# Optimization experiments

Hardware: AMD Instinct MI355X
Metric: run time of the kernel (lower is better)

## Reference

```python
import jax, jax.numpy as jnp
import numpy as np

N = 10000          # nodes
E_RAND = 320000    # random edges (avg degree 32)
F_IN = 512         # nfeat
HID = 256          # args.hid
HEADS = 8          # args.head
FH = HID // HEADS  # 32 per head
NCLASS = 40
TAU = 0.5
LAMDA = 0.5
K = 2


def setup_inputs() -> dict:
    key = jax.random.key(0)
    ks = jax.random.split(key, 16)
    # edge list: random edges + self-loops (so every dst segment is non-empty)
    src = jnp.concatenate([jax.random.randint(ks[0], (E_RAND,), 0, N), jnp.arange(N)])
    dst = jnp.concatenate([jax.random.randint(ks[1], (E_RAND,), 0, N), jnp.arange(N)])
    s = 0.05  # small init scale keeps exp() in attention/bind_loss stable
    return {
        "x": jax.random.normal(ks[2], (N, F_IN), jnp.float32),
        "src": src, "dst": dst,
        "W0": jax.random.normal(ks[3], (F_IN, HEADS, FH), jnp.float32) * s,
        "a0s": jax.random.normal(ks[4], (HEADS, FH), jnp.float32) * s,
        "a0d": jax.random.normal(ks[5], (HEADS, FH), jnp.float32) * s,
        "W1": jax.random.normal(ks[6], (HID, HEADS, FH), jnp.float32) * s,
        "a1s": jax.random.normal(ks[7], (HEADS, FH), jnp.float32) * s,
        "a1d": jax.random.normal(ks[8], (HEADS, FH), jnp.float32) * s,
        "W2": jax.random.normal(ks[9], (HID, HEADS, FH), jnp.float32) * s,
        "a2s": jax.random.normal(ks[10], (HEADS, FH), jnp.float32) * s,
        "a2d": jax.random.normal(ks[11], (HEADS, FH), jnp.float32) * s,
        "Wout": jax.random.normal(ks[12], (HID, HEADS, NCLASS), jnp.float32) * s,
        "aos": jax.random.normal(ks[13], (HEADS, NCLASS), jnp.float32) * s,
        "aod": jax.random.normal(ks[14], (HEADS, NCLASS), jnp.float32) * s,
    }


def _gat_layer(x, W, a_s, a_d, src, dst):
    """Sparse multi-head GAT layer: gather -> edge softmax -> scatter."""
    n = x.shape[0]
    h = jnp.einsum('nf,fhd->nhd', x, W)              # [N,H,Fh]
    es = jnp.sum(h * a_s, axis=-1)                    # [N,H]
    ed = jnp.sum(h * a_d, axis=-1)                    # [N,H]
    e = jax.nn.leaky_relu(es[src] + ed[dst], 0.2)     # [E,H]
    m = jax.ops.segment_max(e, dst, num_segments=n)   # per-dst max (stable softmax)
    w = jnp.exp(e - m[dst])
    z = jax.ops.segment_sum(w, dst, num_segments=n)
    alpha = w / z[dst]                                # [E,H]
    return jax.ops.segment_sum(alpha[:, :, None] * h[src], dst, num_segments=n)  # [N,H,Fh]


def _bind_loss(z):
    # z1 == z2 == z in the original call site: refl_sim == between_sim
    zn = z / jnp.maximum(jnp.linalg.norm(z, axis=1, keepdims=True), 1e-12)
    S = jnp.exp(jnp.matmul(zn, zn.T) / TAU)           # [N,N]
    d = jnp.diagonal(S)
    off = jnp.sum(S, axis=1) - d                      # masked (off-diagonal) row sum
    CT = -jnp.log(d / (off + off))                    # neg_c2.sum + neg_c3.sum
    return jnp.mean(CT)


def reference(x, src, dst, W0, a0s, a0d, W1, a1s, a1d, W2, a2s, a2d, Wout, aos, aod):
    layers = [(W0, a0s, a0d), (W1, a1s, a1d), (W2, a2s, a2d)]
    last = x
    loss = jnp.float32(0.0)
    for i, (W, as_, ad_) in enumerate(layers):
        cur = jax.nn.elu(_gat_layer(last, W, as_, ad_, src, dst))
        cur = cur.reshape(cur.shape[0], -1)           # concat heads -> [N, HID]
        if i > 0:
            beta = LAMDA / (i + 2)                    # MaskLayer(last, cur, lamda, i+2)
            cur = beta * last + (1.0 - beta) * cur
            if i % K == 0:
                loss = loss + _bind_loss(cur)
        last = cur
    out = _gat_layer(last, Wout, aos, aod, src, dst).mean(axis=1)  # avg heads -> [N,C]
    return (jax.nn.log_softmax(out, axis=1), loss)
```

## Files before the change

### kernel.cpp

```cpp
#include <hip/hip_runtime.h>
#include <hip/hip_bf16.h>
#include <math.h>

#define NN_F_IN   512
#define NN_HID    256
#define NN_HEADS  8
#define NN_FH     32
#define NN_NCLASS 40
#define TAU_F     0.5f
#define LAMDA_F   0.5f

typedef __attribute__((ext_vector_type(8))) short bf16x8;
typedef __attribute__((ext_vector_type(4))) float f32x4;

static __device__ __forceinline__ float lrelu02(float x) { return x >= 0.f ? x : 0.2f * x; }
static __device__ __forceinline__ float elu1(float x)    { return x > 0.f ? x : expm1f(x); }
static __device__ __forceinline__ float b2f(unsigned short u) {
    unsigned int x = ((unsigned int)u) << 16;
    return __uint_as_float(x);
}
static __device__ __forceinline__ unsigned short f2b(float f) {
    __hip_bfloat16 hb = __float2bfloat16(f);
    return *reinterpret_cast<unsigned short*>(&hb);
}

__global__ void cast_f2b_kernel(const float* __restrict__ src,
                                unsigned short* __restrict__ dst, int n4) {
    int i = blockIdx.x * 256 + threadIdx.x;
    if (i >= n4) return;
    float4 v = *(const float4*)(src + (size_t)i * 4);
    ushort4 o;
    o.x = f2b(v.x); o.y = f2b(v.y); o.z = f2b(v.z); o.w = f2b(v.w);
    *(ushort4*)(dst + (size_t)i * 4) = o;
}

__global__ void castW_kernel(const float* __restrict__ W, unsigned short* __restrict__ Wt,
                             int K, int Nc, int Np) {
    int idx = blockIdx.x * 256 + threadIdx.x;
    if (idx >= Np * K) return;
    int np = idx / K, k = idx - np * K;
    float v = (np < Nc) ? W[(size_t)k * Nc + np] : 0.f;
    Wt[idx] = f2b(v);
}

__global__ __launch_bounds__(256) void fc_mfma(const unsigned short* __restrict__ A,
                                               const unsigned short* __restrict__ B,
                                               unsigned short* __restrict__ H,
                                               int M, int K, int ncols, int ldH) {
    int t = threadIdx.x, lane = t & 63, wid = t >> 6;
    int wrow = wid >> 1, wcol = wid & 1;
    int l15 = lane & 15, lg = lane >> 4;
    int mbase = blockIdx.y * 64 + wrow * 32;
    int nbase = blockIdx.x * 64 + wcol * 32;

    const unsigned short* Ap[2];
    const unsigned short* Bp[2];
#pragma unroll
    for (int m = 0; m < 2; ++m) {
        int rr = mbase + m * 16 + l15;
        if (rr > M - 1) rr = M - 1;
        Ap[m] = A + (size_t)rr * K + lg * 8;
        Bp[m] = B + (size_t)(nbase + m * 16 + l15) * K + lg * 8;
    }
    f32x4 acc[2][2];
#pragma unroll
    for (int m = 0; m < 2; ++m)
#pragma unroll
        for (int nn = 0; nn < 2; ++nn)
#pragma unroll
            for (int r = 0; r < 4; ++r) acc[m][nn][r] = 0.f;

    bf16x8 aP[2], bP[2], aQ[2], bQ[2];
#pragma unroll
    for (int m = 0; m < 2; ++m) {
        aP[m] = *(const bf16x8*)(Ap[m]);
        bP[m] = *(const bf16x8*)(Bp[m]);
    }
    int nhalf = K >> 6;
    int kk = 32;
    for (int it = 0; it < nhalf; ++it) {
#pragma unroll
        for (int m = 0; m < 2; ++m) {
            aQ[m] = *(const bf16x8*)(Ap[m] + kk);
            bQ[m] = *(const bf16x8*)(Bp[m] + kk);
        }
#pragma unroll
        for (int m = 0; m < 2; ++m)
#pragma unroll
            for (int nn = 0; nn < 2; ++nn)
                acc[m][nn] = __builtin_amdgcn_mfma_f32_16x16x32_bf16(aP[m], bP[nn], acc[m][nn], 0, 0, 0);
        if (it + 1 < nhalf) {
#pragma unroll
            for (int m = 0; m < 2; ++m) {
                aP[m] = *(const bf16x8*)(Ap[m] + kk + 32);
                bP[m] = *(const bf16x8*)(Bp[m] + kk + 32);
            }
        }
#pragma unroll
        for (int m = 0; m < 2; ++m)
#pragma unroll
            for (int nn = 0; nn < 2; ++nn)
                acc[m][nn] = __builtin_amdgcn_mfma_f32_16x16x32_bf16(aQ[m], bQ[nn], acc[m][nn], 0, 0, 0);
        kk += 64;
    }
#pragma unroll
    for (int m = 0; m < 2; ++m) {
#pragma unroll
        for (int nn = 0; nn < 2; ++nn) {
            int col = nbase + nn * 16 + l15;
            if (col >= ncols) continue;
#pragma unroll
            for (int r = 0; r < 4; ++r) {
                int row = mbase + m * 16 + lg * 4 + r;
                if (row < M) H[(size_t)row * ldH + col] = f2b(acc[m][nn][r]);
            }
        }
    }
}

__global__ void attn_kernel(const unsigned short* __restrict__ Hm, const float* __restrict__ As,
                            const float* __restrict__ Ad, float* __restrict__ es,
                            float* __restrict__ ed, int n, int df) {
    int idx = blockIdx.x * blockDim.x + threadIdx.x;
    if (idx >= n * NN_HEADS) return;
    int nn = idx / NN_HEADS, hh = idx - nn * NN_HEADS;
    const unsigned short* hp = Hm + (size_t)nn * NN_HEADS * df + hh * df;
    const float* ap = As + hh * df;
    const float* bp = Ad + hh * df;
    float s1 = 0.f, s2 = 0.f;
    for (int d = 0; d < df; d += 4) {
        ushort4 hv = *(const ushort4*)(hp + d);
        float4 av = *(const float4*)(ap + d);
        float4 bv = *(const float4*)(bp + d);
        float h0 = b2f(hv.x), h1 = b2f(hv.y), h2 = b2f(hv.z), h3 = b2f(hv.w);
        s1 += h0 * av.x + h1 * av.y + h2 * av.z + h3 * av.w;
        s2 += h0 * bv.x + h1 * bv.y + h2 * bv.z + h3 * bv.w;
    }
    es[idx] = s1;
    ed[idx] = s2;
}

__global__ __launch_bounds__(256) void edge_wz(
    const float* __restrict__ es, const float* __restrict__ ed,
    const int* __restrict__ csr_src, const int* __restrict__ row_start,
    float* __restrict__ wC, float* __restrict__ zinv, int n) {
    int lane = threadIdx.x & 63;
    int nn   = blockIdx.x * 4 + (threadIdx.x >> 6);
    if (nn >= n) return;
    int s0 = row_start[nn], s1 = row_start[nn + 1];
    int h    = lane & 7;
    int slot = lane >> 3;
    float edh = ed[nn * NN_HEADS + h];
    float z = 0.f;
    for (int e = s0 + slot; e < s1; e += 8) {
        int sv = csr_src[e];
        float w = expf(lrelu02(es[sv * NN_HEADS + h] + edh));
        wC[(size_t)e * NN_HEADS + h] = w;
        z += w;
    }
    z += __shfl_xor(z, 8, 64);
    z += __shfl_xor(z, 16, 64);
    z += __shfl_xor(z, 32, 64);
    if (slot == 0) zinv[nn * NN_HEADS + h] = 1.f / z;
}

__global__ void count_kernel(const int* __restrict__ dst, int* __restrict__ counts, int E) {
    int e = blockIdx.x * blockDim.x + threadIdx.x;
    if (e < E) atomicAdd(&counts[dst[e]], 1);
}

__global__ void scan_kernel(const int* __restrict__ counts, int* __restrict__ row_start,
                            int* __restrict__ cursor, int n) {
    __shared__ int s[1024];
    int t  = threadIdx.x;
    int ch = (n + 1023) / 1024;
    int lo = t * ch;
    int sum = 0;
    for (int j = 0; j < ch; ++j) {
        int i = lo + j;
        if (i < n) sum += counts[i];
    }
    s[t] = sum;
    __syncthreads();
    for (int off = 1; off < 1024; off <<= 1) {
        int v = 0;
        if (t >= off) v = s[t - off];
        __syncthreads();
        s[t] += v;
        __syncthreads();
    }
    int run = (t == 0) ? 0 : s[t - 1];
    for (int j = 0; j < ch; ++j) {
        int i = lo + j;
        if (i < n) {
            row_start[i] = run;
            cursor[i] = run;
            run += counts[i];
        }
    }
    if (t == 1023) row_start[n] = s[1023];
}

__global__ void scatter_kernel(const int* __restrict__ src, const int* __restrict__ dst,
                               int* __restrict__ cursor, int* __restrict__ csr_src, int E) {
    int e = blockIdx.x * blockDim.x + threadIdx.x;
    if (e < E) {
        int d   = dst[e];
        int pos = atomicAdd(&cursor[d], 1);
        csr_src[pos] = src[e];
    }
}

__global__ __launch_bounds__(256) void gather_hidden(
    const unsigned short* __restrict__ Hm, const float* __restrict__ wC,
    const float* __restrict__ zinv, const int* __restrict__ csr_src,
    const int* __restrict__ row_start, const unsigned short* __restrict__ last,
    unsigned short* __restrict__ out, int n, float beta) {
    int lane = threadIdx.x & 63;
    int nn   = blockIdx.x * 4 + (threadIdx.x >> 6);
    if (nn >= n) return;
    int s0 = row_start[nn], s1 = row_start[nn + 1];
    int h2 = lane >> 3;

    float a0 = 0.f, a1 = 0.f, a2 = 0.f, a3 = 0.f;
    for (int e = s0; e < s1; e += 8) {
        int c = s1 - e;
        int idx[8];
        float wv[8];
#pragma unroll
        for (int j = 0; j < 8; ++j) {
            int p = (j < c) ? e + j : e;
            idx[j] = csr_src[p];
            wv[j]  = wC[(size_t)p * NN_HEADS + h2];
        }
        ushort4 r[8];
#pragma unroll
        for (int j = 0; j < 8; ++j) r[j] = *(const ushort4*)&Hm[(size_t)idx[j] * NN_HID + lane * 4];
#pragma unroll
        for (int j = 0; j < 8; ++j) {
            if (j < c) {
                float w = wv[j];
                a0 += w * b2f(r[j].x); a1 += w * b2f(r[j].y);
                a2 += w * b2f(r[j].z); a3 += w * b2f(r[j].w);
            }
        }
    }
    float zi = zinv[nn * NN_HEADS + h2];
    float v0 = elu1(a0 * zi), v1 = elu1(a1 * zi), v2 = elu1(a2 * zi), v3 = elu1(a3 * zi);
    if (beta >= 0.f) {
        ushort4 lv = *(const ushort4*)&last[(size_t)nn * NN_HID + lane * 4];
        v0 = beta * b2f(lv.x) + (1.f - beta) * v0;
        v1 = beta * b2f(lv.y) + (1.f - beta) * v1;
        v2 = beta * b2f(lv.z) + (1.f - beta) * v2;
        v3 = beta * b2f(lv.w) + (1.f - beta) * v3;
    }
    ushort4 o;
    o.x = f2b(v0); o.y = f2b(v1); o.z = f2b(v2); o.w = f2b(v3);
    *(ushort4*)&out[(size_t)nn * NN_HID + lane * 4] = o;
}

__global__ void gather_final(const unsigned short* __restrict__ Hm, const float* __restrict__ wC,
                             const float* __restrict__ zinv, const int* __restrict__ csr_src,
                             const int* __restrict__ row_start, float* __restrict__ dout, int n) {
    int nn = blockIdx.x;
    __shared__ float accs[NN_HEADS * NN_NCLASS];
    int t = threadIdx.x;
    int s0 = row_start[nn], s1 = row_start[nn + 1];
    int hh = t / NN_NCLASS;
    float acc = 0.f;
    const int LD = NN_HEADS * NN_NCLASS;
    for (int e = s0; e < s1; e += 8) {
        int c = s1 - e;
        int idx[8];
        float wv[8];
#pragma unroll
        for (int j = 0; j < 8; ++j) {
            int p = (j < c) ? e + j : e;
            idx[j] = csr_src[p];
            wv[j]  = wC[(size_t)p * NN_HEADS + hh];
        }
        float v[8];
#pragma unroll
        for (int j = 0; j < 8; ++j) v[j] = b2f(Hm[(size_t)idx[j] * LD + t]);
#pragma unroll
        for (int j = 0; j < 8; ++j) {
            if (j < c) acc += wv[j] * v[j];
        }
    }
    accs[t] = acc * zinv[nn * NN_HEADS + hh];
    __syncthreads();
    if (t < 64) {
        float v = -INFINITY;
        if (t < NN_NCLASS) {
            float sacc = 0.f;
#pragma unroll
            for (int h2 = 0; h2 < NN_HEADS; ++h2) sacc += accs[h2 * NN_NCLASS + t];
            v = sacc * (1.f / NN_HEADS);
        }
        float mx = v;
#pragma unroll
        for (int o = 1; o < 64; o <<= 1) mx = fmaxf(mx, __shfl_xor(mx, o, 64));
        float ex = (t < NN_NCLASS) ? expf(v - mx) : 0.f;
        float se = ex;
#pragma unroll
        for (int o = 1; o < 64; o <<= 1) se += __shfl_xor(se, o, 64);
        if (t < NN_NCLASS) dout[(size_t)nn * NN_NCLASS + t] = (v - mx) - logf(se);
    }
}

__global__ void rownorm_kernel(const unsigned short* __restrict__ z, short* __restrict__ znb,
                               float* __restrict__ dvec, int n) {
    int nn = blockIdx.x;
    int t  = threadIdx.x;
    float v  = b2f(z[(size_t)nn * NN_HID + t]);
    float sq = v * v;
#pragma unroll
    for (int o = 1; o < 64; o <<= 1) sq += __shfl_xor(sq, o, 64);
    __shared__ float ws[4];
    if ((t & 63) == 0) ws[t >> 6] = sq;
    __syncthreads();
    float s = ws[0] + ws[1] + ws[2] + ws[3];
    float m = fmaxf(sqrtf(s), 1e-12f);
    znb[(size_t)nn * NN_HID + t] = (short)f2b(v / m);
    if (t == 0) dvec[nn] = expf((s / (m * m)) * (1.f / TAU_F));
}

__global__ __launch_bounds__(256) void gram_mfma(const short* __restrict__ znb,
                                                 float* __restrict__ P2d, int n,
                                                 int T, int nwg, int Npad) {
    __shared__ short As[128 * 64];
    __shared__ short Bs[128 * 64];

    int b = blockIdx.x;
    int q = nwg >> 3, r8 = nwg & 7, xc = b & 7, oo = b >> 3;
    int sid = (xc < r8 ? xc * (q + 1) : r8 * (q + 1) + (xc - r8) * q) + oo;
    int bi = 0, rem = sid;
    while (rem >= T - bi) { rem -= T - bi; ++bi; }
    int bj = bi + rem;
    int i0 = bi * 128, j0 = bj * 128;

    int t    = threadIdx.x;
    int lane = t & 63;
    int wid  = t >> 6;
    int wrow = wid >> 1, wcol = wid & 1;
    int l15  = lane & 15, lg = lane >> 4;
    int srow = lane >> 3;
    int sch  = lane & 7;

    f32x4 acc[4][4];
#pragma unroll
    for (int m = 0; m < 4; ++m)
#pragma unroll
        for (int nn = 0; nn < 4; ++nn)
#pragma unroll
            for (int r = 0; r < 4; ++r) acc[m][nn][r] = 0.f;

    bf16x8 sa[4], sb[4];
#pragma unroll
    for (int s = 0; s < 4; ++s) {
        int row = wid * 32 + s * 8 + srow;
        int gch = sch ^ (row & 7);
        sa[s] = *(const bf16x8*)(znb + (size_t)(i0 + row) * NN_HID + gch * 8);
        sb[s] = *(const bf16x8*)(znb + (size_t)(j0 + row) * NN_HID + gch * 8);
    }

#pragma unroll
    for (int kt = 0; kt < 4; ++kt) {
#pragma unroll
        for (int s = 0; s < 4; ++s) {
            int row = wid * 32 + s * 8 + srow;
            *(bf16x8*)(&As[row * 64 + sch * 8]) = sa[s];
            *(bf16x8*)(&Bs[row * 64 + sch * 8]) = sb[s];
        }
        __syncthreads();
        if (kt < 3) {
            int kb = (kt + 1) * 64;
#pragma unroll
            for (int s = 0; s < 4; ++s) {
                int row = wid * 32 + s * 8 + srow;
                int gch = sch ^ (row & 7);
                sa[s] = *(const bf16x8*)(znb + (size_t)(i0 + row) * NN_HID + kb + gch * 8);
                sb[s] = *(const bf16x8*)(znb + (size_t)(j0 + row) * NN_HID + kb + gch * 8);
            }
        }
#pragma unroll
        for (int ks = 0; ks < 2; ++ks) {
            bf16x8 av[4], bv[4];
#pragma unroll
            for (int m = 0; m < 4; ++m) {
                int Ra = wrow * 64 + m * 16 + l15;
                int Rb = wcol * 64 + m * 16 + l15;
                int ca = (ks * 4 + lg) ^ (Ra & 7);
                int cb = (ks * 4 + lg) ^ (Rb & 7);
                av[m] = *(const bf16x8*)(&As[Ra * 64 + ca * 8]);
                bv[m] = *(const bf16x8*)(&Bs[Rb * 64 + cb * 8]);
            }
#pragma unroll
            for (int m = 0; m < 4; ++m)
#pragma unroll
                for (int nn = 0; nn < 4; ++nn)
                    acc[m][nn] = __builtin_amdgcn_mfma_f32_16x16x32_bf16(av[m], bv[nn], acc[m][nn], 0, 0, 0);
        }
        __syncthreads();
    }

    int i0w = i0 + wrow * 64;
    int j0w = j0 + wcol * 64;
    bool diag = (bj == bi);
#pragma unroll
    for (int m = 0; m < 4; ++m)
#pragma unroll
        for (int nn = 0; nn < 4; ++nn) {
            int gj = j0w + nn * 16 + l15;
            bool jok = gj < n;
#pragma unroll
            for (int r = 0; r < 4; ++r) {
                int gi = i0w + m * 16 + lg * 4 + r;
                acc[m][nn][r] = (jok && gi < n) ? expf(acc[m][nn][r] * (1.f / TAU_F)) : 0.f;
            }
        }
    float* rowslot = P2d + (size_t)(2 * bj + wcol) * Npad;
#pragma unroll
    for (int m = 0; m < 4; ++m) {
#pragma unroll
        for (int r = 0; r < 4; ++r) {
            float v = acc[m][0][r] + acc[m][1][r] + acc[m][2][r] + acc[m][3][r];
            v += __shfl_xor(v, 1, 64);
            v += __shfl_xor(v, 2, 64);
            v += __shfl_xor(v, 4, 64);
            v += __shfl_xor(v, 8, 64);
            if (l15 == 0) {
                int gi = i0w + m * 16 + lg * 4 + r;
                if (gi < n) rowslot[gi] = v;
            }
        }
    }
    if (!diag) {
        float* colslot = P2d + (size_t)(2 * bi + wrow) * Npad;
#pragma unroll
        for (int nn = 0; nn < 4; ++nn) {
            float v = 0.f;
#pragma unroll
            for (int m = 0; m < 4; ++m)
#pragma unroll
                for (int r = 0; r < 4; ++r) v += acc[m][nn][r];
            v += __shfl_xor(v, 16, 64);
            v += __shfl_xor(v, 32, 64);
            if (lg == 0) {
                int gj = j0w + nn * 16 + l15;
                if (gj < n) colslot[gj] = v;
            }
        }
    }
}

__global__ void fold_kernel(const float* __restrict__ P2d, float* __restrict__ R,
                            int n, int slots, int Npad) {
    int i = blockIdx.x * 256 + threadIdx.x;
    if (i >= n) return;
    const float* p = P2d + i;
    float s0 = 0.f, s1 = 0.f, s2 = 0.f, s3 = 0.f;
    int sl = 0;
    for (; sl + 4 <= slots; sl += 4) {
        s0 += p[(size_t)(sl + 0) * Npad];
        s1 += p[(size_t)(sl + 1) * Npad];
        s2 += p[(size_t)(sl + 2) * Npad];
        s3 += p[(size_t)(sl + 3) * Npad];
    }
    for (; sl < slots; ++sl) s0 += p[(size_t)sl * Npad];
    R[i] = (s0 + s1) + (s2 + s3);
}

__global__ void loss_kernel(const float* __restrict__ R, const float* __restrict__ dvec,
                            float* __restrict__ out_loss, int n) {
    __shared__ float s[1024];
    int t = threadIdx.x;
    float sum = 0.f;
    for (int i = t; i < n; i += 1024) {
        float d   = dvec[i];
        float off = R[i] - d;
        sum += -logf(d / (off + off));
    }
    s[t] = sum;
    __syncthreads();
    for (int o = 512; o > 0; o >>= 1) {
        if (t < o) s[t] += s[t + o];
        __syncthreads();
    }
    if (t == 0) *out_loss = s[0] / n;
}

extern "C" void kernel_launch(void* const* d_in, const int* in_sizes, int n_in,
                              void* d_out, int out_size, void* d_ws, size_t ws_size,
                              hipStream_t stream) {
    const float* x   = (const float*)d_in[0];
    const int*   src = (const int*)d_in[1];
    const int*   dst = (const int*)d_in[2];
    const float* W0  = (const float*)d_in[3];
    const float* a0s = (const float*)d_in[4];
    const float* a0d = (const float*)d_in[5];
    const float* W1  = (const float*)d_in[6];
    const float* a1s = (const float*)d_in[7];
    const float* a1d = (const float*)d_in[8];
    const float* W2  = (const float*)d_in[9];
    const float* a2s = (const float*)d_in[10];
    const float* a2d = (const float*)d_in[11];
    const float* Wout= (const float*)d_in[12];
    const float* aos = (const float*)d_in[13];
    const float* aod = (const float*)d_in[14];

    int N = in_sizes[0] / NN_F_IN;
    int E = in_sizes[1];
    int Npad = ((N + 127) / 128) * 128;
    int T = Npad / 128;
    int nwg = T * (T + 1) / 2;
    float* out = (float*)d_out;

    char*  ws  = (char*)d_ws;
    size_t off = 0;
    auto alloc = [&](size_t bytes) -> void* {
        void* p = ws + off;
        off += bytes;
        off = (off + 255) & ~(size_t)255;
        return p;
    };
    size_t hbBytes = (size_t)N * 320 * 2;
    size_t znBytes = (size_t)Npad * NN_HID * 2;
    unsigned short* Hb = (unsigned short*)alloc(hbBytes > znBytes ? hbBytes : znBytes);
    short* znb = (short*)Hb;
    unsigned short* Bl = (unsigned short*)alloc((size_t)N * NN_HID * 2);
    unsigned short* Bc = (unsigned short*)alloc((size_t)N * NN_HID * 2);
    size_t xbBytes = (size_t)N * NN_F_IN * 2;
    size_t p2Bytes = (size_t)2 * T * Npad * 4;
    void* XbP2d = alloc(xbBytes > p2Bytes ? xbBytes : p2Bytes);
    unsigned short* Xb  = (unsigned short*)XbP2d;
    float*          P2d = (float*)XbP2d;
    unsigned short* Wt0 = (unsigned short*)alloc((size_t)256 * 512 * 2);
    unsigned short* Wt1 = (unsigned short*)alloc((size_t)256 * 256 * 2);
    unsigned short* Wt2 = (unsigned short*)alloc((size_t)256 * 256 * 2);
    unsigned short* Wto = (unsigned short*)alloc((size_t)384 * 256 * 2);
    float* es     = (float*)alloc((size_t)N * NN_HEADS * 4);
    float* ed     = (float*)alloc((size_t)N * NN_HEADS * 4);
    float* wC     = (float*)alloc((size_t)E * NN_HEADS * 4);
    float* zinvA  = (float*)alloc((size_t)N * NN_HEADS * 4);
    float* Rrow   = (float*)alloc((size_t)N * 4);
    float* dvec   = (float*)alloc((size_t)N * 4);
    int*   counts = (int*)alloc((size_t)N * 4);
    int*   rs     = (int*)alloc((size_t)(N + 1) * 4);
    int*   cursor = (int*)alloc((size_t)N * 4);
    int*   csr    = (int*)alloc((size_t)E * 4);

    hipMemsetAsync(counts, 0, (size_t)N * 4, stream);
    count_kernel<<<(E + 255) / 256, 256, 0, stream>>>(dst, counts, E);
    scan_kernel<<<1, 1024, 0, stream>>>(counts, rs, cursor, N);
    scatter_kernel<<<(E + 255) / 256, 256, 0, stream>>>(src, dst, cursor, csr, E);

    cast_f2b_kernel<<<(N * NN_F_IN / 4 + 255) / 256, 256, 0, stream>>>(x, Xb, N * NN_F_IN / 4);
    castW_kernel<<<(256 * 512 + 255) / 256, 256, 0, stream>>>(W0, Wt0, 512, 256, 256);
    castW_kernel<<<(256 * 256 + 255) / 256, 256, 0, stream>>>(W1, Wt1, 256, 256, 256);
    castW_kernel<<<(256 * 256 + 255) / 256, 256, 0, stream>>>(W2, Wt2, 256, 256, 256);
    castW_kernel<<<(384 * 256 + 255) / 256, 256, 0, stream>>>(Wout, Wto, 256, 320, 384);

    int atGrid = (N * NN_HEADS + 255) / 256;
    int ghGrid = (N + 3) / 4;
    int mT64 = (N + 63) / 64;

    fc_mfma<<<dim3(4, mT64), 256, 0, stream>>>(Xb, Wt0, Hb, N, 512, 256, 256);
    attn_kernel<<<atGrid, 256, 0, stream>>>(Hb, a0s, a0d, es, ed, N, NN_FH);
    edge_wz<<<ghGrid, 256, 0, stream>>>(es, ed, csr, rs, wC, zinvA, N);
    gather_hidden<<<ghGrid, 256, 0, stream>>>(Hb, wC, zinvA, csr, rs, nullptr, Bl, N, -1.f);

    fc_mfma<<<dim3(4, mT64), 256, 0, stream>>>(Bl, Wt1, Hb, N, 256, 256, 256);
    attn_kernel<<<atGrid, 256, 0, stream>>>(Hb, a1s, a1d, es, ed, N, NN_FH);
    edge_wz<<<ghGrid, 256, 0, stream>>>(es, ed, csr, rs, wC, zinvA, N);
    gather_hidden<<<ghGrid, 256, 0, stream>>>(Hb, wC, zinvA, csr, rs, Bl, Bc, N, LAMDA_F / 3.f);

    fc_mfma<<<dim3(4, mT64), 256, 0, stream>>>(Bc, Wt2, Hb, N, 256, 256, 256);
    attn_kernel<<<atGrid, 256, 0, stream>>>(Hb, a2s, a2d, es, ed, N, NN_FH);
    edge_wz<<<ghGrid, 256, 0, stream>>>(es, ed, csr, rs, wC, zinvA, N);
    gather_hidden<<<ghGrid, 256, 0, stream>>>(Hb, wC, zinvA, csr, rs, Bc, Bl, N, LAMDA_F / 4.f);

    rownorm_kernel<<<N, 256, 0, stream>>>(Bl, znb, dvec, N);
    hipMemsetAsync(znb + (size_t)N * NN_HID, 0, (size_t)(Npad - N) * NN_HID * 2, stream);
    hipMemsetAsync(P2d, 0, (size_t)2 * T * Npad * 4, stream);
    gram_mfma<<<nwg, 256, 0, stream>>>(znb, P2d, N, T, nwg, Npad);
    fold_kernel<<<(N + 255) / 256, 256, 0, stream>>>(P2d, Rrow, N, 2 * T, Npad);
    loss_kernel<<<1, 1024, 0, stream>>>(Rrow, dvec, out + (size_t)N * NN_NCLASS, N);

    fc_mfma<<<dim3(5, mT64), 256, 0, stream>>>(Bl, Wto, Hb, N, 256, 320, 320);
    attn_kernel<<<atGrid, 256, 0, stream>>>(Hb, aos, aod, es, ed, N, NN_NCLASS);
    edge_wz<<<ghGrid, 256, 0, stream>>>(es, ed, csr, rs, wC, zinvA, N);
    gather_final<<<N, NN_HEADS * NN_NCLASS, 0, stream>>>(Hb, wC, zinvA, csr, rs, out, N);
}
```

Baseline: 432.9 us.

## Fuse cast kernels, use fast exp, and widen gram K-tile to 128

Merges the five input/weight cast kernels into one prep kernel to cut launch overhead. Replaces expf with __expf in the edge weight, row-norm and gram epilogue paths. Doubles the gram kernel's shared-memory K tile from 64 to 128, halving the K iterations and barriers at the cost of twice the LDS per block, which may lower occupancy. Fast exp trades a little accuracy.

```diff
diff --git a/kernel.cpp b/kernel.cpp
--- a/kernel.cpp
+++ b/kernel.cpp
@@ -24,23 +24,44 @@
     return *reinterpret_cast<unsigned short*>(&hb);
 }
 
-__global__ void cast_f2b_kernel(const float* __restrict__ src,
-                                unsigned short* __restrict__ dst, int n4) {
+__global__ void prep_kernel(const float* __restrict__ x,
+                            const float* __restrict__ W0, const float* __restrict__ W1,
+                            const float* __restrict__ W2, const float* __restrict__ Wo,
+                            unsigned short* __restrict__ Xb,
+                            unsigned short* __restrict__ Wt0, unsigned short* __restrict__ Wt1,
+                            unsigned short* __restrict__ Wt2, unsigned short* __restrict__ Wto,
+                            int n4X) {
     int i = blockIdx.x * 256 + threadIdx.x;
-    if (i >= n4) return;
-    float4 v = *(const float4*)(src + (size_t)i * 4);
-    ushort4 o;
-    o.x = f2b(v.x); o.y = f2b(v.y); o.z = f2b(v.z); o.w = f2b(v.w);
-    *(ushort4*)(dst + (size_t)i * 4) = o;
-}
-
-__global__ void castW_kernel(const float* __restrict__ W, unsigned short* __restrict__ Wt,
-                             int K, int Nc, int Np) {
-    int idx = blockIdx.x * 256 + threadIdx.x;
-    if (idx >= Np * K) return;
-    int np = idx / K, k = idx - np * K;
-    float v = (np < Nc) ? W[(size_t)k * Nc + np] : 0.f;
-    Wt[idx] = f2b(v);
+    if (i < n4X) {
+        float4 v = *(const float4*)(x + (size_t)i * 4);
+        ushort4 o;
+        o.x = f2b(v.x); o.y = f2b(v.y); o.z = f2b(v.z); o.w = f2b(v.w);
+        *(ushort4*)(Xb + (size_t)i * 4) = o;
+        return;
+    }
+    i -= n4X;
+    if (i < 256 * 512) {
+        int np = i >> 9, k = i & 511;
+        Wt0[i] = f2b(W0[(size_t)k * 256 + np]);
+        return;
+    }
+    i -= 256 * 512;
+    if (i < 256 * 256) {
+        int np = i >> 8, k = i & 255;
+        Wt1[i] = f2b(W1[(size_t)k * 256 + np]);
+        return;
+    }
+    i -= 256 * 256;
+    if (i < 256 * 256) {
+        int np = i >> 8, k = i & 255;
+        Wt2[i] = f2b(W2[(size_t)k * 256 + np]);
+        return;
+    }
+    i -= 256 * 256;
+    if (i < 384 * 256) {
+        int np = i >> 8, k = i & 255;
+        Wto[i] = f2b(np < 320 ? Wo[(size_t)k * 320 + np] : 0.f);
+    }
 }
 
 __global__ __launch_bounds__(256) void fc_mfma(const unsigned short* __restrict__ A,
@@ -154,7 +175,7 @@
     float z = 0.f;
     for (int e = s0 + slot; e < s1; e += 8) {
         int sv = csr_src[e];
-        float w = expf(lrelu02(es[sv * NN_HEADS + h] + edh));
+        float w = __expf(lrelu02(es[sv * NN_HEADS + h] + edh));
         wC[(size_t)e * NN_HEADS + h] = w;
         z += w;
     }
@@ -322,14 +343,14 @@
     float s = ws[0] + ws[1] + ws[2] + ws[3];
     float m = fmaxf(sqrtf(s), 1e-12f);
     znb[(size_t)nn * NN_HID + t] = (short)f2b(v / m);
-    if (t == 0) dvec[nn] = expf((s / (m * m)) * (1.f / TAU_F));
+    if (t == 0) dvec[nn] = __expf((s / (m * m)) * (1.f / TAU_F));
 }
 
 __global__ __launch_bounds__(256) void gram_mfma(const short* __restrict__ znb,
                                                  float* __restrict__ P2d, int n,
                                                  int T, int nwg, int Npad) {
-    __shared__ short As[128 * 64];
-    __shared__ short Bs[128 * 64];
+    __shared__ short As[128 * 128];
+    __shared__ short Bs[128 * 128];
 
     int b = blockIdx.x;
     int q = nwg >> 3, r8 = nwg & 7, xc = b & 7, oo = b >> 3;
@@ -344,8 +365,8 @@
     int wid  = t >> 6;
     int wrow = wid >> 1, wcol = wid & 1;
     int l15  = lane & 15, lg = lane >> 4;
-    int srow = lane >> 3;
-    int sch  = lane & 7;
+    int sc16 = lane & 15;
+    int sr4  = lane >> 4;
 
     f32x4 acc[4][4];
 #pragma unroll
@@ -355,36 +376,35 @@
 #pragma unroll
             for (int r = 0; r < 4; ++r) acc[m][nn][r] = 0.f;
 
-    bf16x8 sa[4], sb[4];
-#pragma unroll
-    for (int s = 0; s < 4; ++s) {
-        int row = wid * 32 + s * 8 + srow;
-        int gch = sch ^ (row & 7);
+    bf16x8 sa[8], sb[8];
+#pragma unroll
+    for (int s = 0; s < 8; ++s) {
+        int row = wid * 32 + sr4 * 8 + s;
+        int gch = sc16 ^ (row & 7);
         sa[s] = *(const bf16x8*)(znb + (size_t)(i0 + row) * NN_HID + gch * 8);
         sb[s] = *(const bf16x8*)(znb + (size_t)(j0 + row) * NN_HID + gch * 8);
     }
 
 #pragma unroll
-    for (int kt = 0; kt < 4; ++kt) {
-#pragma unroll
-        for (int s = 0; s < 4; ++s) {
-            int row = wid * 32 + s * 8 + srow;
-            *(bf16x8*)(&As[row * 64 + sch * 8]) = sa[s];
-            *(bf16x8*)(&Bs[row * 64 + sch * 8]) = sb[s];
+    for (int kt = 0; kt < 2; ++kt) {
+#pragma unroll
+        for (int s = 0; s < 8; ++s) {
+            int row = wid * 32 + sr4 * 8 + s;
+            *(bf16x8*)(&As[row * 128 + sc16 * 8]) = sa[s];
+            *(bf16x8*)(&Bs[row * 128 + sc16 * 8]) = sb[s];
         }
         __syncthreads();
-        if (kt < 3) {
-            int kb = (kt + 1) * 64;
-#pragma unroll
-            for (int s = 0; s < 4; ++s) {
-                int row = wid * 32 + s * 8 + srow;
-                int gch = sch ^ (row & 7);
-                sa[s] = *(const bf16x8*)(znb + (size_t)(i0 + row) * NN_HID + kb + gch * 8);
-                sb[s] = *(const bf16x8*)(znb + (size_t)(j0 + row) * NN_HID + kb + gch * 8);
-            }
-        }
-#pragma unroll
-        for (int ks = 0; ks < 2; ++ks) {
+        if (kt == 0) {
+#pragma unroll
+            for (int s = 0; s < 8; ++s) {
+                int row = wid * 32 + sr4 * 8 + s;
+                int gch = sc16 ^ (row & 7);
+                sa[s] = *(const bf16x8*)(znb + (size_t)(i0 + row) * NN_HID + 128 + gch * 8);
+                sb[s] = *(const bf16x8*)(znb + (size_t)(j0 + row) * NN_HID + 128 + gch * 8);
+            }
+        }
+#pragma unroll
+        for (int ks = 0; ks < 4; ++ks) {
             bf16x8 av[4], bv[4];
 #pragma unroll
             for (int m = 0; m < 4; ++m) {
@@ -392,8 +412,8 @@
                 int Rb = wcol * 64 + m * 16 + l15;
                 int ca = (ks * 4 + lg) ^ (Ra & 7);
                 int cb = (ks * 4 + lg) ^ (Rb & 7);
-                av[m] = *(const bf16x8*)(&As[Ra * 64 + ca * 8]);
-                bv[m] = *(const bf16x8*)(&Bs[Rb * 64 + cb * 8]);
+                av[m] = *(const bf16x8*)(&As[Ra * 128 + ca * 8]);
+                bv[m] = *(const bf16x8*)(&Bs[Rb * 128 + cb * 8]);
             }
 #pragma unroll
             for (int m = 0; m < 4; ++m)
@@ -401,7 +421,7 @@
                 for (int nn = 0; nn < 4; ++nn)
                     acc[m][nn] = __builtin_amdgcn_mfma_f32_16x16x32_bf16(av[m], bv[nn], acc[m][nn], 0, 0, 0);
         }
-        __syncthreads();
+        if (kt == 0) __syncthreads();
     }
 
     int i0w = i0 + wrow * 64;
@@ -416,7 +436,7 @@
 #pragma unroll
             for (int r = 0; r < 4; ++r) {
                 int gi = i0w + m * 16 + lg * 4 + r;
-                acc[m][nn][r] = (jok && gi < n) ? expf(acc[m][nn][r] * (1.f / TAU_F)) : 0.f;
+                acc[m][nn][r] = (jok && gi < n) ? __expf(acc[m][nn][r] * (1.f / TAU_F)) : 0.f;
             }
         }
     float* rowslot = P2d + (size_t)(2 * bj + wcol) * Npad;
@@ -555,11 +575,10 @@
     scan_kernel<<<1, 1024, 0, stream>>>(counts, rs, cursor, N);
     scatter_kernel<<<(E + 255) / 256, 256, 0, stream>>>(src, dst, cursor, csr, E);
 
-    cast_f2b_kernel<<<(N * NN_F_IN / 4 + 255) / 256, 256, 0, stream>>>(x, Xb, N * NN_F_IN / 4);
-    castW_kernel<<<(256 * 512 + 255) / 256, 256, 0, stream>>>(W0, Wt0, 512, 256, 256);
-    castW_kernel<<<(256 * 256 + 255) / 256, 256, 0, stream>>>(W1, Wt1, 256, 256, 256);
-    castW_kernel<<<(256 * 256 + 255) / 256, 256, 0, stream>>>(W2, Wt2, 256, 256, 256);
-    castW_kernel<<<(384 * 256 + 255) / 256, 256, 0, stream>>>(Wout, Wto, 256, 320, 384);
+    int n4X = N * NN_F_IN / 4;
+    int prepTotal = n4X + 256 * 512 + 256 * 256 + 256 * 256 + 384 * 256;
+    prep_kernel<<<(prepTotal + 255) / 256, 256, 0, stream>>>(
+        x, W0, W1, W2, Wout, Xb, Wt0, Wt1, Wt2, Wto, n4X);
 
     int atGrid = (N * NN_HEADS + 255) / 256;
     int ghGrid = (N + 3) / 4;
```

After: 415.1 us. 1.04x faster.
